# Kernel tuning notes

Hardware: AMD Instinct MI355X
Metric: run time of the kernel (lower is better)

Reference implementation:

```python
import jax, jax.numpy as jnp
import numpy as np

B, T, V, H, W = 2, 4, 4, 128, 128
NQ = 64
QDIM, IDIM, MDIM = 256, 32, 16

def setup_inputs() -> dict:
    key = jax.random.key(0)
    ks = jax.random.split(key, 9)
    return {
        "instance_affinity": jax.random.normal(ks[0], (B, T, V, H, W, IDIM), dtype=jnp.float32),
        "motion_code": jax.random.normal(ks[1], (B, T, V, H, W, MDIM), dtype=jnp.float32),
        "query_feat": jax.random.normal(ks[2], (B, T, NQ, QDIM), dtype=jnp.float32),
        "assignment_prob": jax.random.uniform(ks[3], (B, T, V, H, W, NQ + 1), dtype=jnp.float32),
        "assigned_query": jax.random.randint(ks[4], (B, T, V, H, W), 0, NQ + 1, dtype=jnp.int64),
        "W_inst": jax.random.normal(ks[5], (QDIM, IDIM), dtype=jnp.float32) * 0.02,
        "b_inst": jax.random.normal(ks[6], (IDIM,), dtype=jnp.float32) * 0.02,
        "W_motion": jax.random.normal(ks[7], (QDIM, MDIM), dtype=jnp.float32) * 0.02,
        "b_motion": jax.random.normal(ks[8], (MDIM,), dtype=jnp.float32) * 0.02,
    }

def reference(instance_affinity, motion_code, query_feat, assignment_prob, assigned_query, W_inst, b_inst, W_motion, b_motion):
    # project queries: (b,t,q,query_dim) -> (b,t,q,d)
    query_inst = query_feat @ W_inst + b_inst      # (b,t,q,32)
    query_motion = query_feat @ W_motion + b_motion  # (b,t,q,16)
    bg_prob = assignment_prob[..., :1]   # (b,t,v,h,w,1)
    fg_prob = assignment_prob[..., 1:]   # (b,t,v,h,w,nq)
    fg_norm = jnp.maximum(fg_prob.sum(axis=-1, keepdims=True), 1e-6)
    # weighted-sum pooling over queries as a fused contraction (no huge broadcast intermediate)
    pooled_inst = jnp.einsum('btvhwq,btqd->btvhwd', fg_prob, query_inst) / fg_norm
    pooled_motion = jnp.einsum('btvhwq,btqd->btvhwd', fg_prob, query_motion) / fg_norm
    refine_gate = 1.0 - bg_prob
    inst = instance_affinity + refine_gate * pooled_inst
    motion = motion_code + refine_gate * pooled_motion
    entity_id = assigned_query  # already (b,t,v,h,w)
    return (entity_id, inst, motion)
```

## Files before the change

kernel.cpp:

```cpp
#include <hip/hip_runtime.h>

#define BT    8
#define VHW   (4*128*128)
#define NQn   64
#define QD    256
#define ID    32
#define MD    16
#define CD    48
#define APW   65
#define PITCH 72

typedef short bf16x8 __attribute__((ext_vector_type(8)));
typedef float f32x4  __attribute__((ext_vector_type(4)));

static __device__ __forceinline__ short f2bf(float f) {
    unsigned u = __builtin_bit_cast(unsigned, f);
    unsigned r = (u + 0x7FFFu + ((u >> 16) & 1u)) >> 16;
    return (short)r;
}

__global__ __launch_bounds__(256) void qproj_kernel(
    const float* __restrict__ qf,
    const float* __restrict__ Wi,
    const float* __restrict__ bi,
    const float* __restrict__ Wm,
    const float* __restrict__ bm,
    short* __restrict__ qtabB)
{
    int idx = blockIdx.x * 256 + threadIdx.x;
    int btq = idx / CD;
    int d   = idx - btq * CD;
    int bt  = btq >> 6;
    int q   = btq & 63;
    const float* __restrict__ qrow = qf + btq * QD;
    float a;
    if (d < ID) {
        a = bi[d];
        #pragma unroll 8
        for (int k = 0; k < QD; ++k) a = fmaf(qrow[k], Wi[k*ID + d], a);
    } else {
        int dm = d - ID;
        a = bm[dm];
        #pragma unroll 8
        for (int k = 0; k < QD; ++k) a = fmaf(qrow[k], Wm[k*MD + dm], a);
    }
    int nt = d >> 4, c = d & 15;
    int kt = q >> 5, kk = q & 31;
    int lane = ((kk >> 3) << 4) | c;
    int j    = kk & 7;
    qtabB[((((bt*3 + nt)*2 + kt) << 6) + lane) * 8 + j] = f2bf(a);
}

__global__ __launch_bounds__(256) void entity_kernel(
    const float* __restrict__ ia,
    const float* __restrict__ mc,
    const float* __restrict__ ap,
    const int*   __restrict__ aq,
    const short* __restrict__ qtabB,
    float* __restrict__ out_id,
    float* __restrict__ out_inst,
    float* __restrict__ out_mot)
{
    __shared__ short ap_s[256 * PITCH];
    __shared__ float bg_s[256];
    __shared__ float psum_s[256];
    __shared__ float scale_s[256];

    const int  t    = threadIdx.x;
    const int  lane = t & 63;
    const int  w    = t >> 6;
    const int  bt   = blockIdx.x >> 8;
    const long base = (long)blockIdx.x << 8;

    {
        const float4* __restrict__ src = (const float4*)(ap + base * APW);
        #pragma unroll
        for (int k = 0; k < 17; ++k) {
            int f = t + 256 * k;
            if (f < (256 * APW) / 4) {
                float4 v = src[f];
                int e0 = 4 * f;
                #pragma unroll
                for (int e = 0; e < 4; ++e) {
                    int   ix  = e0 + e;
                    int   loc = ix / APW;
                    int   col = ix - loc * APW;
                    float val = (&v.x)[e];
                    if (col == 0) bg_s[loc] = val;
                    else          ap_s[loc * PITCH + (col - 1)] = f2bf(val);
                }
            }
        }
    }

    bf16x8 Bf[3][2];
    {
        const bf16x8* __restrict__ qb = (const bf16x8*)(qtabB + bt * (3*2*64*8));
        #pragma unroll
        for (int nt = 0; nt < 3; ++nt)
            #pragma unroll
            for (int kt = 0; kt < 2; ++kt)
                Bf[nt][kt] = qb[(nt*2 + kt) * 64 + lane];
    }
    bf16x8 Bones;
    {
        short one = ((lane & 15) == 0) ? (short)0x3F80 : (short)0;
        #pragma unroll
        for (int j = 0; j < 8; ++j) Bones[j] = one;
    }

    __syncthreads();

    f32x4 acc[4][3];
    f32x4 accP[4];
    #pragma unroll
    for (int m = 0; m < 4; ++m) {
        accP[m] = (f32x4){0.f, 0.f, 0.f, 0.f};
        #pragma unroll
        for (int n = 0; n < 3; ++n) acc[m][n] = (f32x4){0.f, 0.f, 0.f, 0.f};
    }
    #pragma unroll
    for (int kt = 0; kt < 2; ++kt) {
        #pragma unroll
        for (int m = 0; m < 4; ++m) {
            const bf16x8 A = *(const bf16x8*)(ap_s +
                (w*64 + m*16 + (lane & 15)) * PITCH + kt*32 + ((lane >> 4) << 3));
            acc[m][0] = __builtin_amdgcn_mfma_f32_16x16x32_bf16(A, Bf[0][kt], acc[m][0], 0, 0, 0);
            acc[m][1] = __builtin_amdgcn_mfma_f32_16x16x32_bf16(A, Bf[1][kt], acc[m][1], 0, 0, 0);
            acc[m][2] = __builtin_amdgcn_mfma_f32_16x16x32_bf16(A, Bf[2][kt], acc[m][2], 0, 0, 0);
            accP[m]   = __builtin_amdgcn_mfma_f32_16x16x32_bf16(A, Bones,     accP[m],   0, 0, 0);
        }
    }

    if ((lane & 15) == 0) {
        int g = lane >> 4;
        #pragma unroll
        for (int m = 0; m < 4; ++m)
            #pragma unroll
            for (int r = 0; r < 4; ++r)
                psum_s[w*64 + m*16 + g*4 + r] = accP[m][r];
    }
    __syncthreads();
    scale_s[t] = (1.0f - bg_s[t]) / fmaxf(psum_s[t], 1e-6f);
    __syncthreads();

    const int c = lane & 15, g = lane >> 4;
    #pragma unroll
    for (int m = 0; m < 4; ++m) {
        const int lrow = w*64 + m*16 + g*4;
        #pragma unroll
        for (int r = 0; r < 4; ++r) {
            const long  loc = base + lrow + r;
            const float s   = scale_s[lrow + r];
            out_inst[loc*ID + c]      = ia[loc*ID + c]      + s * acc[m][0][r];
            out_inst[loc*ID + 16 + c] = ia[loc*ID + 16 + c] + s * acc[m][1][r];
            out_mot [loc*MD + c]      = mc[loc*MD + c]      + s * acc[m][2][r];
        }
    }
    out_id[base + t] = (float)aq[base + t];
}

extern "C" void kernel_launch(void* const* d_in, const int* in_sizes, int n_in,
                              void* d_out, int out_size, void* d_ws, size_t ws_size,
                              hipStream_t stream) {
    const float* ia = (const float*)d_in[0];
    const float* mc = (const float*)d_in[1];
    const float* qf = (const float*)d_in[2];
    const float* ap = (const float*)d_in[3];
    const int*   aq = (const int*)  d_in[4];
    const float* Wi = (const float*)d_in[5];
    const float* bi = (const float*)d_in[6];
    const float* Wm = (const float*)d_in[7];
    const float* bm = (const float*)d_in[8];

    short* qtabB = (short*)d_ws;

    float* out_id   = (float*)d_out;
    float* out_inst = out_id + (long)BT * VHW;
    float* out_mot  = out_inst + (long)BT * VHW * ID;

    qproj_kernel<<<(BT * NQn * CD) / 256, 256, 0, stream>>>(qf, Wi, bi, Wm, bm, qtabB);
    entity_kernel<<<(BT * VHW) / 256, 256, 0, stream>>>(ia, mc, ap, aq, qtabB,
                                                        out_id, out_inst, out_mot);
}
```

Before: 341.4 us.

## Halve block tile, stage raw fp32 probs in LDS and coalesce output stores

Each block now handles 128 locations instead of 256. The assignment probabilities are copied into shared memory as raw float4 values with no per-element divide or modulo, and the conversion to bf16 happens when the MFMA A operands are read. The ia and mc inputs are prefetched as coalesced float4 loads before the barrier. Results are staged in shared memory so the outputs can be written as coalesced float4 stores. This aims to remove the costly scatter during the load and the strided 64-byte global accesses, at the cost of more LDS traffic, unaligned 65-float-stride reads that may cause bank conflicts, and extra barriers.

```diff
diff --git a/kernel.cpp b/kernel.cpp
--- a/kernel.cpp
+++ b/kernel.cpp
@@ -1,14 +1,15 @@
 #include <hip/hip_runtime.h>
 
-#define BT    8
-#define VHW   (4*128*128)
-#define NQn   64
-#define QD    256
-#define ID    32
-#define MD    16
-#define CD    48
-#define APW   65
-#define PITCH 72
+#define BT     8
+#define VHW    (4*128*128)
+#define NQn    64
+#define QD     256
+#define ID     32
+#define MD     16
+#define CD     48
+#define APW    65
+#define LOCS   128
+#define PPITCH 52
 
 typedef short bf16x8 __attribute__((ext_vector_type(8)));
 typedef float f32x4  __attribute__((ext_vector_type(4)));
@@ -51,7 +52,7 @@
     qtabB[((((bt*3 + nt)*2 + kt) << 6) + lane) * 8 + j] = f2bf(a);
 }
 
-__global__ __launch_bounds__(256) void entity_kernel(
+__global__ __launch_bounds__(256, 4) void entity_kernel(
     const float* __restrict__ ia,
     const float* __restrict__ mc,
     const float* __restrict__ ap,
@@ -61,36 +62,22 @@
     float* __restrict__ out_inst,
     float* __restrict__ out_mot)
 {
-    __shared__ short ap_s[256 * PITCH];
-    __shared__ float bg_s[256];
-    __shared__ float psum_s[256];
-    __shared__ float scale_s[256];
+    __shared__ __align__(16) float smem[LOCS * APW];
+    __shared__ float psum_s[LOCS];
+    __shared__ float scale_s[LOCS];
 
     const int  t    = threadIdx.x;
     const int  lane = t & 63;
     const int  w    = t >> 6;
-    const int  bt   = blockIdx.x >> 8;
-    const long base = (long)blockIdx.x << 8;
+    const int  bt   = blockIdx.x >> 9;
+    const long base = (long)blockIdx.x * LOCS;
 
     {
         const float4* __restrict__ src = (const float4*)(ap + base * APW);
-        #pragma unroll
-        for (int k = 0; k < 17; ++k) {
-            int f = t + 256 * k;
-            if (f < (256 * APW) / 4) {
-                float4 v = src[f];
-                int e0 = 4 * f;
-                #pragma unroll
-                for (int e = 0; e < 4; ++e) {
-                    int   ix  = e0 + e;
-                    int   loc = ix / APW;
-                    int   col = ix - loc * APW;
-                    float val = (&v.x)[e];
-                    if (col == 0) bg_s[loc] = val;
-                    else          ap_s[loc * PITCH + (col - 1)] = f2bf(val);
-                }
-            }
-        }
+        float4* __restrict__ dst = (float4*)smem;
+        #pragma unroll
+        for (int k = 0; k < 8; ++k) dst[t + 256 * k] = src[t + 256 * k];
+        if (t < (LOCS * APW / 4 - 2048)) dst[2048 + t] = src[2048 + t];
     }
 
     bf16x8 Bf[3][2];
@@ -109,12 +96,25 @@
         for (int j = 0; j < 8; ++j) Bones[j] = one;
     }
 
-    __syncthreads();
-
-    f32x4 acc[4][3];
-    f32x4 accP[4];
-    #pragma unroll
-    for (int m = 0; m < 4; ++m) {
+    float4 ia_r[4], mc_r[2];
+    float  idv = 0.f;
+    {
+        const float4* __restrict__ ia4 = (const float4*)(ia + base * ID);
+        const float4* __restrict__ mc4 = (const float4*)(mc + base * MD);
+        #pragma unroll
+        for (int k = 0; k < 4; ++k) ia_r[k] = ia4[t + 256 * k];
+        #pragma unroll
+        for (int k = 0; k < 2; ++k) mc_r[k] = mc4[t + 256 * k];
+        if (t < LOCS) idv = (float)aq[base + t];
+    }
+
+    __syncthreads();
+
+    const int c = lane & 15, g = lane >> 4;
+    f32x4 acc[2][3];
+    f32x4 accP[2];
+    #pragma unroll
+    for (int m = 0; m < 2; ++m) {
         accP[m] = (f32x4){0.f, 0.f, 0.f, 0.f};
         #pragma unroll
         for (int n = 0; n < 3; ++n) acc[m][n] = (f32x4){0.f, 0.f, 0.f, 0.f};
@@ -122,9 +122,11 @@
     #pragma unroll
     for (int kt = 0; kt < 2; ++kt) {
         #pragma unroll
-        for (int m = 0; m < 4; ++m) {
-            const bf16x8 A = *(const bf16x8*)(ap_s +
-                (w*64 + m*16 + (lane & 15)) * PITCH + kt*32 + ((lane >> 4) << 3));
+        for (int m = 0; m < 2; ++m) {
+            const float* __restrict__ ar = smem + (w*32 + m*16 + c) * APW + 1 + kt*32 + g*8;
+            bf16x8 A;
+            #pragma unroll
+            for (int j = 0; j < 8; ++j) A[j] = f2bf(ar[j]);
             acc[m][0] = __builtin_amdgcn_mfma_f32_16x16x32_bf16(A, Bf[0][kt], acc[m][0], 0, 0, 0);
             acc[m][1] = __builtin_amdgcn_mfma_f32_16x16x32_bf16(A, Bf[1][kt], acc[m][1], 0, 0, 0);
             acc[m][2] = __builtin_amdgcn_mfma_f32_16x16x32_bf16(A, Bf[2][kt], acc[m][2], 0, 0, 0);
@@ -132,32 +134,53 @@
         }
     }
 
-    if ((lane & 15) == 0) {
-        int g = lane >> 4;
-        #pragma unroll
-        for (int m = 0; m < 4; ++m)
+    if (c == 0) {
+        #pragma unroll
+        for (int m = 0; m < 2; ++m)
             #pragma unroll
             for (int r = 0; r < 4; ++r)
-                psum_s[w*64 + m*16 + g*4 + r] = accP[m][r];
-    }
-    __syncthreads();
-    scale_s[t] = (1.0f - bg_s[t]) / fmaxf(psum_s[t], 1e-6f);
-    __syncthreads();
-
-    const int c = lane & 15, g = lane >> 4;
-    #pragma unroll
-    for (int m = 0; m < 4; ++m) {
-        const int lrow = w*64 + m*16 + g*4;
+                psum_s[w*32 + m*16 + g*4 + r] = accP[m][r];
+    }
+    __syncthreads();
+    if (t < LOCS)
+        scale_s[t] = (1.0f - smem[t * APW]) / fmaxf(psum_s[t], 1e-6f);
+    __syncthreads();
+
+    #pragma unroll
+    for (int m = 0; m < 2; ++m) {
+        const int lrow = w*32 + m*16 + g*4;
         #pragma unroll
         for (int r = 0; r < 4; ++r) {
-            const long  loc = base + lrow + r;
-            const float s   = scale_s[lrow + r];
-            out_inst[loc*ID + c]      = ia[loc*ID + c]      + s * acc[m][0][r];
-            out_inst[loc*ID + 16 + c] = ia[loc*ID + 16 + c] + s * acc[m][1][r];
-            out_mot [loc*MD + c]      = mc[loc*MD + c]      + s * acc[m][2][r];
+            const float s  = scale_s[lrow + r];
+            const int   po = (lrow + r) * PPITCH;
+            smem[po + c]      = s * acc[m][0][r];
+            smem[po + 16 + c] = s * acc[m][1][r];
+            smem[po + 32 + c] = s * acc[m][2][r];
         }
     }
-    out_id[base + t] = (float)aq[base + t];
+    __syncthreads();
+
+    float4* __restrict__ oi4 = (float4*)(out_inst + base * ID);
+    float4* __restrict__ om4 = (float4*)(out_mot  + base * MD);
+    #pragma unroll
+    for (int k = 0; k < 4; ++k) {
+        int i = t + 256 * k;
+        int loc = i >> 3, d4 = i & 7;
+        const float* p = smem + loc * PPITCH + d4 * 4;
+        float4 v = ia_r[k];
+        v.x += p[0]; v.y += p[1]; v.z += p[2]; v.w += p[3];
+        oi4[i] = v;
+    }
+    #pragma unroll
+    for (int k = 0; k < 2; ++k) {
+        int i = t + 256 * k;
+        int loc = i >> 2, d4 = i & 3;
+        const float* p = smem + loc * PPITCH + 32 + d4 * 4;
+        float4 v = mc_r[k];
+        v.x += p[0]; v.y += p[1]; v.z += p[2]; v.w += p[3];
+        om4[i] = v;
+    }
+    if (t < LOCS) out_id[base + t] = idv;
 }
 
 extern "C" void kernel_launch(void* const* d_in, const int* in_sizes, int n_in,
@@ -180,6 +203,6 @@
     float* out_mot  = out_inst + (long)BT * VHW * ID;
 
     qproj_kernel<<<(BT * NQn * CD) / 256, 256, 0, stream>>>(qf, Wi, bi, Wm, bm, qtabB);
-    entity_kernel<<<(BT * VHW) / 256, 256, 0, stream>>>(ia, mc, ap, aq, qtabB,
-                                                        out_id, out_inst, out_mot);
-}
+    entity_kernel<<<(BT * VHW) / LOCS, 256, 0, stream>>>(ia, mc, ap, aq, qtabB,
+                                                         out_id, out_inst, out_mot);
+}
```

Result: faster. 329.8 us (-3.4%).
